# Optimization experiments

Measured on AMD Instinct MI355X. Metric: run time of the kernel, lower is better.

The kernel has to match this reference:

```python
import jax, jax.numpy as jnp
import numpy as np

N_NODES = 100000
N_EDGES = 400000
N_GRAPHS = 2500
DIM = 128
F_IN = 78
N_LAYERS = 3
BN_EPS = 1e-5


def setup_inputs() -> dict:
    key = jax.random.key(0)
    ks = jax.random.split(key, 24)
    def lin(k, fi, fo):
        return jax.random.normal(k, (fi, fo), jnp.float32) / np.sqrt(fi)
    inp = {
        "x": jax.random.normal(ks[0], (N_NODES, F_IN), jnp.float32),
        "edge_index": jax.random.randint(ks[1], (2, N_EDGES), 0, N_NODES, jnp.int32),
        "batch": jnp.sort(jax.random.randint(ks[2], (N_NODES,), 0, N_GRAPHS, jnp.int32)),
        "num_graphs": N_GRAPHS,
        "gcn1_W": lin(ks[3], F_IN, DIM), "gcn1_b": jnp.zeros((DIM,), jnp.float32),
        "gcn2_W": lin(ks[4], DIM, DIM), "gcn2_b": jnp.zeros((DIM,), jnp.float32),
        "gin0_w1": lin(ks[5], F_IN, DIM), "gin0_b1": jnp.zeros((DIM,), jnp.float32),
        "gin0_w2": lin(ks[6], DIM, DIM), "gin0_b2": jnp.zeros((DIM,), jnp.float32),
        # layers 1..2 stacked (same 128->128 shapes)
        "gin_w1": jnp.stack([lin(ks[7], DIM, DIM), lin(ks[8], DIM, DIM)]),
        "gin_b1": jnp.zeros((2, DIM), jnp.float32),
        "gin_w2": jnp.stack([lin(ks[9], DIM, DIM), lin(ks[10], DIM, DIM)]),
        "gin_b2": jnp.zeros((2, DIM), jnp.float32),
        "bn_gamma": jnp.ones((N_LAYERS, DIM), jnp.float32),
        "bn_beta": jnp.zeros((N_LAYERS, DIM), jnp.float32),
    }
    return inp


def reference(x, edge_index, batch, num_graphs,
              gcn1_W, gcn1_b, gcn2_W, gcn2_b,
              gin0_w1, gin0_b1, gin0_w2, gin0_b2,
              gin_w1, gin_b1, gin_w2, gin_b2,
              bn_gamma, bn_beta):
    n = x.shape[0]
    src, dst = edge_index[0], edge_index[1]

    def gcn(h, W, b):
        # linear -> symmetric-normalized aggregation with self loops (PyG GCNConv)
        h = h @ W
        loop = jnp.arange(n, dtype=src.dtype)
        s = jnp.concatenate([src, loop])
        d = jnp.concatenate([dst, loop])
        deg = jax.ops.segment_sum(jnp.ones(s.shape[0], h.dtype), d, num_segments=n)
        dis = jax.lax.rsqrt(deg)  # deg >= 1 thanks to self loops
        norm = (dis[s] * dis[d])[:, None]
        return jax.ops.segment_sum(h[s] * norm, d, num_segments=n) + b

    def gin(h, w1, b1, w2, b2):
        # GINConv, eps=0: mlp(x + sum_{j->i} x_j)
        agg = jax.ops.segment_sum(h[src], dst, num_segments=n)
        z = jax.nn.relu((h + agg) @ w1 + b1)
        return z @ w2 + b2

    def bn(h, g, bt):
        mu = h.mean(0)
        var = ((h - mu) ** 2).mean(0)
        return (h - mu) * jax.lax.rsqrt(var + BN_EPS) * g + bt

    g1 = jax.nn.relu(gcn(x, gcn1_W, gcn1_b))
    g2 = jax.nn.relu(gcn(g1, gcn2_W, gcn2_b))
    g2a = g2 + g1
    g2m = g2 * g1

    h = x
    xs = []
    m = jnp.float32(1.0)
    e = jnp.float32(0.0)
    for i in range(N_LAYERS):
        if i == 0:
            h = gin(h, gin0_w1, gin0_b1, gin0_w2, gin0_b2)
        else:
            h = gin(h, gin_w1[i - 1], gin_b1[i - 1], gin_w2[i - 1], gin_b2[i - 1])
        h = bn(jax.nn.relu(h), bn_gamma[i], bn_beta[i])
        m = m * h
        e = e + h
        xs.append(h)

    rep = jnp.concatenate(xs + [m, e, g1, g2, g2a, g2m], axis=-1)  # [N, 9*DIM]
    return jax.ops.segment_max(rep, batch, num_segments=num_graphs)
```

## Files before the change

### kernel.cpp

```cpp
#include <hip/hip_runtime.h>
#include <math.h>

#define DIMC 128
#define FINC 78
#define REPW 1152
#define SCAN_TILE 1024

typedef __attribute__((ext_vector_type(8))) short short8x;
typedef __attribute__((ext_vector_type(4))) float f32x4;
typedef unsigned int u32;
typedef const __attribute__((address_space(1))) u32* gas_u32p;
typedef __attribute__((address_space(3))) u32* las_u32p;

__device__ inline float b2f(unsigned short u) {
    union { unsigned int i; float f; } v; v.i = ((unsigned int)u) << 16; return v.f;
}
__device__ inline unsigned short f2b(float f) {
    union { float f; unsigned int i; } v; v.f = f;
    unsigned int r = (v.i + 0x7FFFu + ((v.i >> 16) & 1u)) >> 16;
    return (unsigned short)r;
}

__device__ __forceinline__ void gld16(const void* g, void* l) {
    __builtin_amdgcn_global_load_lds((gas_u32p)g, (las_u32p)l, 16, 0, 0);
}


__global__ void k_fill_int(int* __restrict__ p, int v, int n) {
    int i = blockIdx.x * blockDim.x + threadIdx.x;
    if (i < n) p[i] = v;
}

__global__ void k_fill(float* __restrict__ p, float v, int n) {
    int i = blockIdx.x * blockDim.x + threadIdx.x;
    if (i < n) p[i] = v;
}

__global__ void k_count(const int* __restrict__ dst, int* __restrict__ cnt, int E) {
    int e = blockIdx.x * blockDim.x + threadIdx.x;
    if (e < E) atomicAdd(&cnt[dst[e]], 1);
}

__launch_bounds__(256)
__global__ void k_tilesum(const int* __restrict__ cnt, int* __restrict__ tileSum, int N) {
    __shared__ int red[256];
    int base = blockIdx.x * SCAN_TILE;
    int s = 0;
    for (int i = threadIdx.x; i < SCAN_TILE; i += 256) {
        int idx = base + i;
        if (idx < N) s += cnt[idx];
    }
    red[threadIdx.x] = s;
    __syncthreads();
    for (int d = 128; d > 0; d >>= 1) {
        if (threadIdx.x < d) red[threadIdx.x] += red[threadIdx.x + d];
        __syncthreads();
    }
    if (threadIdx.x == 0) tileSum[blockIdx.x] = red[0];
}

__launch_bounds__(256)
__global__ void k_tilescan(const int* __restrict__ tileSum, int* __restrict__ tileOff,
                           int* __restrict__ rowptr, int T, int N) {
    __shared__ int sh[256];
    int t = threadIdx.x;
    int orig = (t < T) ? tileSum[t] : 0;
    sh[t] = orig;
    __syncthreads();
    for (int d = 1; d < 256; d <<= 1) {
        int v = (t >= d) ? sh[t - d] : 0;
        __syncthreads();
        sh[t] += v;
        __syncthreads();
    }
    if (t < T) tileOff[t] = sh[t] - orig;
    if (t == 255) rowptr[N] = sh[255];
}

__launch_bounds__(256)
__global__ void k_tileemit(const int* __restrict__ cnt, const int* __restrict__ tileOff,
                           int* __restrict__ rowptr, int* __restrict__ cursor,
                           float* __restrict__ dis, int N) {
    __shared__ int sh[256];
    int t = threadIdx.x;
    int base = blockIdx.x * SCAN_TILE;
    int idx0 = base + t * 4;
    int v0 = 0, v1 = 0, v2 = 0, v3 = 0;
    if (idx0 + 3 < N) {
        int4 v = *(const int4*)(cnt + idx0);
        v0 = v.x; v1 = v.y; v2 = v.z; v3 = v.w;
    } else {
        if (idx0 + 0 < N) v0 = cnt[idx0 + 0];
        if (idx0 + 1 < N) v1 = cnt[idx0 + 1];
        if (idx0 + 2 < N) v2 = cnt[idx0 + 2];
        if (idx0 + 3 < N) v3 = cnt[idx0 + 3];
    }
    int s0 = v0, s1 = s0 + v1, s2 = s1 + v2, s3 = s2 + v3;
    sh[t] = s3;
    __syncthreads();
    for (int d = 1; d < 256; d <<= 1) {
        int v = (t >= d) ? sh[t - d] : 0;
        __syncthreads();
        sh[t] += v;
        __syncthreads();
    }
    int gbase = tileOff[blockIdx.x] + ((t == 0) ? 0 : sh[t - 1]);
    int ex[4] = {0, s0, s1, s2};
    int vv[4] = {v0, v1, v2, v3};
#pragma unroll
    for (int j = 0; j < 4; ++j) {
        int idx = idx0 + j;
        if (idx < N) {
            int r = gbase + ex[j];
            rowptr[idx] = r;
            cursor[idx] = r;
            dis[idx] = rsqrtf((float)vv[j] + 1.0f);
        }
    }
}

__global__ void k_scatter(const int* __restrict__ src, const int* __restrict__ dst,
                          int* __restrict__ cursor, int* __restrict__ col, int E) {
    int e = blockIdx.x * blockDim.x + threadIdx.x;
    if (e < E) {
        int pos = atomicAdd(&cursor[dst[e]], 1);
        col[pos] = src[e];
    }
}

__global__ void k_bounds(const int* __restrict__ batch, int* __restrict__ start, int N, int G) {
    int g = blockIdx.x * blockDim.x + threadIdx.x;
    if (g <= G) {
        int lo = 0, hi = N;
        while (lo < hi) { int mid = (lo + hi) >> 1; if (batch[mid] < g) lo = mid + 1; else hi = mid; }
        start[g] = lo;
    }
}


__global__ void k_cvt_w(const float* __restrict__ s0, const float* __restrict__ s1,
                        const float* __restrict__ s2, const float* __restrict__ s3,
                        const float* __restrict__ s4, const float* __restrict__ s5,
                        const float* __restrict__ s6, const float* __restrict__ s7,
                        unsigned short* __restrict__ whi, unsigned short* __restrict__ wlo) {
    int my = blockIdx.y;
    const float* src; int Ksrc, KP; size_t dstoff;
    const size_t o96 = (size_t)128 * 96, o128 = (size_t)128 * 128;
    switch (my) {
        case 0: src = s0; Ksrc = 78;  KP = 96;  dstoff = 0; break;
        case 1: src = s1; Ksrc = 78;  KP = 96;  dstoff = o96; break;
        case 2: src = s2; Ksrc = 128; KP = 128; dstoff = 2 * o96; break;
        case 3: src = s3; Ksrc = 128; KP = 128; dstoff = 2 * o96 + o128; break;
        case 4: src = s4; Ksrc = 128; KP = 128; dstoff = 2 * o96 + 2 * o128; break;
        case 5: src = s5; Ksrc = 128; KP = 128; dstoff = 2 * o96 + 3 * o128; break;
        case 6: src = s6; Ksrc = 128; KP = 128; dstoff = 2 * o96 + 4 * o128; break;
        default: src = s7; Ksrc = 128; KP = 128; dstoff = 2 * o96 + 5 * o128; break;
    }
    int i = blockIdx.x * blockDim.x + threadIdx.x;
    if (i < 128 * KP) {
        int n = i / KP, k = i - n * KP;
        float v = (k < Ksrc) ? src[(size_t)k * DIMC + n] : 0.f;
        unsigned short hi = f2b(v);
        unsigned short lo = f2b(v - b2f(hi));
        whi[dstoff + i] = hi;
        wlo[dstoff + i] = lo;
    }
}


__global__ void k_pad_x(const float* __restrict__ x, float* __restrict__ x96, int N) {
    int i = blockIdx.x * blockDim.x + threadIdx.x;
    int r = i / 24, c4 = (i - r * 24) * 4;
    if (r >= N) return;
    float v[4];
#pragma unroll
    for (int j = 0; j < 4; ++j) { int k = c4 + j; v[j] = (k < FINC) ? x[(size_t)r * FINC + k] : 0.f; }
    *(float4*)(x96 + (size_t)r * 96 + c4) = make_float4(v[0], v[1], v[2], v[3]);
}


__launch_bounds__(256, 2)
__global__ void k_gemm_x2(const float* __restrict__ A,
                          const unsigned short* __restrict__ B0hi, const unsigned short* __restrict__ B0lo,
                          const unsigned short* __restrict__ B1hi, const unsigned short* __restrict__ B1lo,
                          const float* __restrict__ rowScale0,
                          float* __restrict__ C0, float* __restrict__ C1, int N) {
    constexpr int KP = 96, NC = 3;
    __shared__ float          ldsA[NC * 4096];
    __shared__ unsigned short ldsB[2][4096];
    const int tid = threadIdx.x;
    const int wave = tid >> 6, lane = tid & 63;
    const int lm = lane & 15, q = lane >> 4;
    const int wr = (wave >> 1) * 64, wc = (wave & 1) * 64;
    const int row0 = blockIdx.x * 128;

    const int au = tid & 7, ar = tid >> 3;
    const int bu = tid & 3, br = tid >> 2;

#pragma unroll
    for (int c = 0; c < NC; ++c)
#pragma unroll
        for (int p = 0; p < 4; ++p) {
            int r = p * 32 + ar;
            gld16(A + (size_t)(row0 + r) * KP + c * 32 + ((au ^ (r & 7)) << 2),
                  &ldsA[((c * 4 + p) * 256 + tid) << 2]);
        }

    const unsigned short* bh2[2] = {B0hi, B1hi};
    const unsigned short* bl2[2] = {B0lo, B1lo};

#pragma unroll
    for (int ws = 0; ws < 2; ++ws) {
        f32x4 acc[4][4];
#pragma unroll
        for (int a = 0; a < 4; ++a)
#pragma unroll
            for (int b = 0; b < 4; ++b) acc[a][b] = (f32x4){0.f, 0.f, 0.f, 0.f};

#pragma unroll
        for (int c = 0; c < NC; ++c) {
#pragma unroll
            for (int p = 0; p < 2; ++p) {
                int r = p * 64 + br;
                int so = (c << 5) + ((bu ^ ((r >> 1) & 3)) << 3);
                gld16(bh2[ws] + (size_t)r * KP + so, &ldsB[0][(p * 256 + tid) << 3]);
                gld16(bl2[ws] + (size_t)r * KP + so, &ldsB[1][(p * 256 + tid) << 3]);
            }
            asm volatile("s_waitcnt vmcnt(0)" ::: "memory");
            __builtin_amdgcn_s_barrier();
            __builtin_amdgcn_sched_barrier(0);

            short8x ah[4], al[4];
#pragma unroll
            for (int rt = 0; rt < 4; ++rt) {
                int m = wr + rt * 16 + lm;
                const float* base = &ldsA[c * 4096];
                float4 f0 = *(const float4*)&base[m * 32 + (((2 * q) ^ (m & 7)) << 2)];
                float4 f1 = *(const float4*)&base[m * 32 + ((((2 * q) + 1) ^ (m & 7)) << 2)];
                float ff[8] = {f0.x, f0.y, f0.z, f0.w, f1.x, f1.y, f1.z, f1.w};
#pragma unroll
                for (int j = 0; j < 8; ++j) {
                    unsigned short h = f2b(ff[j]);
                    ah[rt][j] = (short)h;
                    al[rt][j] = (short)f2b(ff[j] - b2f(h));
                }
            }
#pragma unroll
            for (int ct = 0; ct < 4; ++ct) {
                int n = wc + ct * 16 + lm;
                int sl = n * 32 + ((q ^ ((n >> 1) & 3)) << 3);
                short8x bh = *(const short8x*)&ldsB[0][sl];
                short8x bl = *(const short8x*)&ldsB[1][sl];
#pragma unroll
                for (int rt = 0; rt < 4; ++rt) {
                    acc[rt][ct] = __builtin_amdgcn_mfma_f32_16x16x32_bf16(bh, ah[rt], acc[rt][ct], 0, 0, 0);
                    acc[rt][ct] = __builtin_amdgcn_mfma_f32_16x16x32_bf16(bh, al[rt], acc[rt][ct], 0, 0, 0);
                    acc[rt][ct] = __builtin_amdgcn_mfma_f32_16x16x32_bf16(bl, ah[rt], acc[rt][ct], 0, 0, 0);
                }
            }
            __builtin_amdgcn_s_barrier();
        }

        float* C = ws ? C1 : C0;
#pragma unroll
        for (int rt = 0; rt < 4; ++rt) {
            int grow = row0 + wr + rt * 16 + lm;
            if (grow < N) {
                float sc = ws ? 1.f : rowScale0[grow];
#pragma unroll
                for (int ct = 0; ct < 4; ++ct) {
                    int nb = wc + ct * 16 + q * 4;
                    *(float4*)(C + (size_t)grow * DIMC + nb) =
                        make_float4(acc[rt][ct][0] * sc, acc[rt][ct][1] * sc,
                                    acc[rt][ct][2] * sc, acc[rt][ct][3] * sc);
                }
            }
        }
    }
}


template<int KP, bool STATS>
__launch_bounds__(256, 2)
__global__ void k_gemm_c(const float* __restrict__ A,
                         const unsigned short* __restrict__ Bhi,
                         const unsigned short* __restrict__ Blo,
                         const float* __restrict__ bias, const float* __restrict__ rowScale,
                         float* __restrict__ statsOut, float* __restrict__ C,
                         int N, int doRelu) {
    constexpr int NT = KP / 32;
    __shared__ float          ldsA[2][4096];
    __shared__ unsigned short ldsB[2][2][4096];
    __shared__ float sStats[256];
    const int tid = threadIdx.x;
    const int wave = tid >> 6, lane = tid & 63;
    const int lm = lane & 15, q = lane >> 4;
    const int wr = (wave >> 1) * 64, wc = (wave & 1) * 64;
    const int row0 = blockIdx.x * 128;

    const int au = tid & 7, ar = tid >> 3;
    const int bu = tid & 3, br = tid >> 2;

    auto stage = [&](int c, int d) {
        const int cb = c << 5;
#pragma unroll
        for (int p = 0; p < 4; ++p) {
            int r = p * 32 + ar;
            gld16(A + (size_t)(row0 + r) * KP + cb + ((au ^ (r & 7)) << 2),
                  &ldsA[d][(p * 256 + tid) << 2]);
        }
#pragma unroll
        for (int p = 0; p < 2; ++p) {
            int r = p * 64 + br;
            int so = cb + ((bu ^ ((r >> 1) & 3)) << 3);
            gld16(Bhi + (size_t)r * KP + so, &ldsB[d][0][(p * 256 + tid) << 3]);
            gld16(Blo + (size_t)r * KP + so, &ldsB[d][1][(p * 256 + tid) << 3]);
        }
    };

    f32x4 acc[4][4];
#pragma unroll
    for (int a = 0; a < 4; ++a)
#pragma unroll
        for (int b = 0; b < 4; ++b) acc[a][b] = (f32x4){0.f, 0.f, 0.f, 0.f};

    stage(0, 0);
#pragma unroll
    for (int t = 0; t < NT; ++t) {
        const int cur = t & 1;
        if (t + 1 < NT) {
            stage(t + 1, cur ^ 1);
            asm volatile("s_waitcnt vmcnt(8)" ::: "memory");
        } else {
            asm volatile("s_waitcnt vmcnt(0)" ::: "memory");
        }
        __builtin_amdgcn_s_barrier();
        __builtin_amdgcn_sched_barrier(0);

        short8x ah[4], al[4];
#pragma unroll
        for (int rt = 0; rt < 4; ++rt) {
            int m = wr + rt * 16 + lm;
            float4 f0 = *(const float4*)&ldsA[cur][m * 32 + (((2 * q) ^ (m & 7)) << 2)];
            float4 f1 = *(const float4*)&ldsA[cur][m * 32 + ((((2 * q) + 1) ^ (m & 7)) << 2)];
            float ff[8] = {f0.x, f0.y, f0.z, f0.w, f1.x, f1.y, f1.z, f1.w};
#pragma unroll
            for (int j = 0; j < 8; ++j) {
                unsigned short h = f2b(ff[j]);
                ah[rt][j] = (short)h;
                al[rt][j] = (short)f2b(ff[j] - b2f(h));
            }
        }
#pragma unroll
        for (int ct = 0; ct < 4; ++ct) {
            int n = wc + ct * 16 + lm;
            int sl = n * 32 + ((q ^ ((n >> 1) & 3)) << 3);
            short8x bh = *(const short8x*)&ldsB[cur][0][sl];
            short8x bl = *(const short8x*)&ldsB[cur][1][sl];
#pragma unroll
            for (int rt = 0; rt < 4; ++rt) {
                acc[rt][ct] = __builtin_amdgcn_mfma_f32_16x16x32_bf16(bh, ah[rt], acc[rt][ct], 0, 0, 0);
                acc[rt][ct] = __builtin_amdgcn_mfma_f32_16x16x32_bf16(bh, al[rt], acc[rt][ct], 0, 0, 0);
                acc[rt][ct] = __builtin_amdgcn_mfma_f32_16x16x32_bf16(bl, ah[rt], acc[rt][ct], 0, 0, 0);
            }
        }
        __builtin_amdgcn_s_barrier();
    }

    float cs[4][4], cq[4][4];
    if constexpr (STATS) {
#pragma unroll
        for (int a = 0; a < 4; ++a)
#pragma unroll
            for (int b = 0; b < 4; ++b) { cs[a][b] = 0.f; cq[a][b] = 0.f; }
    }

#pragma unroll
    for (int rt = 0; rt < 4; ++rt) {
        int grow = row0 + wr + rt * 16 + lm;
        if (grow < N) {
            float sc = rowScale ? rowScale[grow] : 1.f;
#pragma unroll
            for (int ct = 0; ct < 4; ++ct) {
                int nb = wc + ct * 16 + q * 4;
                float vv[4];
#pragma unroll
                for (int i = 0; i < 4; ++i) {
                    float v = acc[rt][ct][i];
                    if (bias) v += bias[nb + i];
                    if (doRelu) v = fmaxf(v, 0.f);
                    v *= sc;
                    vv[i] = v;
                    if constexpr (STATS) { cs[ct][i] += v; cq[ct][i] = fmaf(v, v, cq[ct][i]); }
                }
                *(float4*)(C + (size_t)grow * DIMC + nb) = make_float4(vv[0], vv[1], vv[2], vv[3]);
            }
        }
    }

    if constexpr (STATS) {
        sStats[tid] = 0.f;
        __syncthreads();
#pragma unroll
        for (int ct = 0; ct < 4; ++ct)
#pragma unroll
            for (int i = 0; i < 4; ++i) {
                float vs = cs[ct][i], vq = cq[ct][i];
#pragma unroll
                for (int o = 1; o < 16; o <<= 1) { vs += __shfl_xor(vs, o); vq += __shfl_xor(vq, o); }
                if (lm == 0) {
                    int colg = wc + ct * 16 + q * 4 + i;
                    atomicAdd(&sStats[colg], vs);
                    atomicAdd(&sStats[DIMC + colg], vq);
                }
            }
        __syncthreads();
        atomicAdd(&statsOut[tid], sStats[tid]);
    }
}


__global__ void k_bn_coef(const float* __restrict__ bnsum, const float* __restrict__ gamma,
                          const float* __restrict__ beta, float* __restrict__ coef, float invN) {
    int c = threadIdx.x;
    float mu  = bnsum[c] * invN;
    float var = bnsum[128 + c] * invN - mu * mu;
    float inv = rsqrtf(var + 1e-5f);
    float s = gamma[c] * inv;
    coef[c] = s;
    coef[128 + c] = beta[c] - mu * s;
}


__global__ void k_fold_w(const float* __restrict__ w1, const float* __restrict__ coefL,
                         unsigned short* __restrict__ fwhi, unsigned short* __restrict__ fwlo,
                         float* __restrict__ cvec) {
    __shared__ float red[128];
    int n = blockIdx.x, k = threadIdx.x;
    float w = w1[(size_t)k * DIMC + n];
    float ws = w * coefL[k];
    unsigned short h = f2b(ws);
    fwhi[(size_t)n * DIMC + k] = h;
    fwlo[(size_t)n * DIMC + k] = f2b(ws - b2f(h));
    red[k] = w * coefL[DIMC + k];
    __syncthreads();
    for (int d = 64; d > 0; d >>= 1) { if (k < d) red[k] += red[k + d]; __syncthreads(); }
    if (k == 0) cvec[n] = red[0];
}


__global__ void k_gather_gcn(const float4* __restrict__ t, const int* __restrict__ rowptr,
                             const int* __restrict__ col, const float* __restrict__ dis,
                             const float4* __restrict__ bias, float4* __restrict__ out, int N) {
    int i = blockIdx.x * blockDim.x + threadIdx.x;
    int node = i >> 5, c4 = i & 31;
    if (node >= N) return;
    int s = rowptr[node], e = rowptr[node + 1];
    float4 acc = t[(size_t)node * 32 + c4];
    for (int k = s; k < e; ++k) {
        float4 v = t[(size_t)col[k] * 32 + c4];
        acc.x += v.x; acc.y += v.y; acc.z += v.z; acc.w += v.w;
    }
    float d = dis[node];
    float4 b = bias[c4];
    float4 o;
    o.x = fmaxf(acc.x * d + b.x, 0.f);
    o.y = fmaxf(acc.y * d + b.y, 0.f);
    o.z = fmaxf(acc.z * d + b.z, 0.f);
    o.w = fmaxf(acc.w * d + b.w, 0.f);
    out[(size_t)node * 32 + c4] = o;
}

__global__ void k_gather_gin(const float4* __restrict__ t, const int* __restrict__ rowptr,
                             const int* __restrict__ col, const float4* __restrict__ bias,
                             float4* __restrict__ out, int N) {
    int i = blockIdx.x * blockDim.x + threadIdx.x;
    int node = i >> 5, c4 = i & 31;
    if (node >= N) return;
    int s = rowptr[node], e = rowptr[node + 1];
    float4 acc = t[(size_t)node * 32 + c4];
    for (int k = s; k < e; ++k) {
        float4 v = t[(size_t)col[k] * 32 + c4];
        acc.x += v.x; acc.y += v.y; acc.z += v.z; acc.w += v.w;
    }
    float4 b = bias[c4];
    float4 o;
    o.x = fmaxf(acc.x + b.x, 0.f);
    o.y = fmaxf(acc.y + b.y, 0.f);
    o.z = fmaxf(acc.z + b.z, 0.f);
    o.w = fmaxf(acc.w + b.w, 0.f);
    out[(size_t)node * 32 + c4] = o;
}


__global__ void k_segmax_gin_all(const float* __restrict__ h0, const float* __restrict__ h1,
                                 const float* __restrict__ h2, const float* __restrict__ coef,
                                 const int* __restrict__ start, float* __restrict__ out) {
    int g = blockIdx.x, c = threadIdx.x;
    float s0 = coef[c],       t0 = coef[128 + c];
    float s1 = coef[256 + c], t1 = coef[384 + c];
    float s2 = coef[512 + c], t2 = coef[640 + c];
    int s = start[g], e = start[g + 1];
    float m0 = -INFINITY, m1 = -INFINITY, m2 = -INFINITY, mm = -INFINITY, me = -INFINITY;
    for (int n = s; n < e; ++n) {
        size_t idx = (size_t)n * DIMC + c;
        float a0 = fmaf(h0[idx], s0, t0);
        float a1 = fmaf(h1[idx], s1, t1);
        float a2 = fmaf(h2[idx], s2, t2);
        m0 = fmaxf(m0, a0); m1 = fmaxf(m1, a1); m2 = fmaxf(m2, a2);
        mm = fmaxf(mm, a0 * a1 * a2);
        me = fmaxf(me, a0 + a1 + a2);
    }
    size_t o = (size_t)g * REPW + c;
    out[o]            = m0;
    out[o + 1 * DIMC] = m1;
    out[o + 2 * DIMC] = m2;
    out[o + 3 * DIMC] = mm;
    out[o + 4 * DIMC] = me;
}

__global__ void k_segmax_gcn(const float* __restrict__ G1, const float* __restrict__ G2,
                             const int* __restrict__ start, float* __restrict__ out) {
    int g = blockIdx.x, c = threadIdx.x;
    int s = start[g], e = start[g + 1];
    float m1 = -INFINITY, m2 = -INFINITY, ma = -INFINITY, mm = -INFINITY;
    for (int n = s; n < e; ++n) {
        float a = G1[(size_t)n * DIMC + c], b = G2[(size_t)n * DIMC + c];
        m1 = fmaxf(m1, a); m2 = fmaxf(m2, b);
        ma = fmaxf(ma, a + b); mm = fmaxf(mm, a * b);
    }
    size_t o = (size_t)g * REPW + c;
    out[o + 5 * DIMC] = m1;
    out[o + 6 * DIMC] = m2;
    out[o + 7 * DIMC] = ma;
    out[o + 8 * DIMC] = mm;
}


extern "C" void kernel_launch(void* const* d_in, const int* in_sizes, int n_in,
                              void* d_out, int out_size, void* d_ws, size_t ws_size,
                              hipStream_t stream) {
    const float* x       = (const float*)d_in[0];
    const int*   ei      = (const int*)d_in[1];
    const int*   batch   = (const int*)d_in[2];
    const float* gcn1_W  = (const float*)d_in[4];
    const float* gcn1_b  = (const float*)d_in[5];
    const float* gcn2_W  = (const float*)d_in[6];
    const float* gcn2_b  = (const float*)d_in[7];
    const float* gin0_w1 = (const float*)d_in[8];
    const float* gin0_b1 = (const float*)d_in[9];
    const float* gin0_w2 = (const float*)d_in[10];
    const float* gin0_b2 = (const float*)d_in[11];
    const float* gin_w1  = (const float*)d_in[12];
    const float* gin_b1  = (const float*)d_in[13];
    const float* gin_w2  = (const float*)d_in[14];
    const float* gin_b2  = (const float*)d_in[15];
    const float* bn_g    = (const float*)d_in[16];
    const float* bn_b    = (const float*)d_in[17];
    float* out = (float*)d_out;

    const int N = in_sizes[0] / FINC;
    const int E = in_sizes[1] / 2;
    const int G = out_size / REPW;
    const int* srcv = ei;
    const int* dstv = ei + E;

    char* ws = (char*)d_ws;
    size_t off = 0;
    auto alloc = [&](size_t bytes) { char* p = ws + off; off += (bytes + 255) & ~(size_t)255; return p; };
    int*   cnt     = (int*)alloc((size_t)N * 4);
    int*   rowptr  = (int*)alloc(((size_t)N + 1) * 4);
    int*   cursor  = (int*)alloc((size_t)N * 4);
    int*   col     = (int*)alloc((size_t)E * 4);
    float* dis     = (float*)alloc((size_t)N * 4);
    float* bnsum   = (float*)alloc(768 * 4);
    float* coef    = (float*)alloc(768 * 4);
    float* cvec    = (float*)alloc(128 * 4);
    int*   start   = (int*)alloc(((size_t)G + 1) * 4);
    int*   tileSum = (int*)alloc(256 * 4);
    int*   tileOff = (int*)alloc(256 * 4);
    const size_t o96 = (size_t)128 * 96, o128 = (size_t)128 * 128;
    const size_t wtElems = 2 * o96 + 6 * o128;
    unsigned short* whi  = (unsigned short*)alloc(wtElems * 2);
    unsigned short* wlo  = (unsigned short*)alloc(wtElems * 2);
    unsigned short* fwhi = (unsigned short*)alloc(o128 * 2);
    unsigned short* fwlo = (unsigned short*)alloc(o128 * 2);
    const size_t fbytes = (size_t)N * DIMC * 4;
    float* bufT = (float*)alloc(fbytes);
    float* bufZ = (float*)alloc(fbytes);
    float* h0   = (float*)alloc(fbytes);
    float* h1   = (float*)alloc(fbytes);
    float* h2   = (float*)alloc(fbytes);
    float* x96  = h1;
    (void)ws_size; (void)n_in;

    const size_t woff[8] = {0, o96, 2 * o96, 2 * o96 + o128, 2 * o96 + 2 * o128,
                            2 * o96 + 3 * o128, 2 * o96 + 4 * o128, 2 * o96 + 5 * o128};

    const int T = 256;
    auto cdiv = [](long a, long b) { return (int)((a + b - 1) / b); };
    const int gemmGrid = cdiv(N, 128);
    const int gatherGrid = cdiv((long)N * 32, T);
    const int nTiles = cdiv(N, SCAN_TILE);
    const float invN = 1.0f / (float)N;

    k_fill_int<<<cdiv(N, T), T, 0, stream>>>(cnt, 0, N);
    k_count<<<cdiv(E, T), T, 0, stream>>>(dstv, cnt, E);
    k_tilesum<<<nTiles, T, 0, stream>>>(cnt, tileSum, N);
    k_tilescan<<<1, T, 0, stream>>>(tileSum, tileOff, rowptr, nTiles, N);
    k_tileemit<<<nTiles, T, 0, stream>>>(cnt, tileOff, rowptr, cursor, dis, N);
    k_scatter<<<cdiv(E, T), T, 0, stream>>>(srcv, dstv, cursor, col, E);
    k_bounds<<<cdiv(G + 1, T), T, 0, stream>>>(batch, start, N, G);
    k_fill<<<3, T, 0, stream>>>(bnsum, 0.f, 768);
    {
        dim3 g(64, 8);
        k_cvt_w<<<g, T, 0, stream>>>(gcn1_W, gin0_w1, gcn2_W, gin0_w2,
                                     gin_w1, gin_w1 + o128, gin_w2, gin_w2 + o128, whi, wlo);
    }
    k_pad_x<<<cdiv((long)N * 24, T), T, 0, stream>>>(x, x96, N);

    k_gemm_x2<<<gemmGrid, T, 0, stream>>>(x96, whi + woff[0], wlo + woff[0],
                                          whi + woff[1], wlo + woff[1],
                                          dis, bufT, h2, N);

    k_gather_gcn<<<gatherGrid, T, 0, stream>>>((const float4*)bufT, rowptr, col, dis,
                                               (const float4*)gcn1_b, (float4*)bufZ, N);
    k_gemm_c<128, false><<<gemmGrid, T, 0, stream>>>(bufZ, whi + woff[2], wlo + woff[2],
                                                     nullptr, dis, nullptr, bufT, N, 0);
    k_gather_gcn<<<gatherGrid, T, 0, stream>>>((const float4*)bufT, rowptr, col, dis,
                                               (const float4*)gcn2_b, (float4*)h0, N);
    k_segmax_gcn<<<G, DIMC, 0, stream>>>(bufZ, h0, start, out);

    k_gather_gin<<<gatherGrid, T, 0, stream>>>((const float4*)h2, rowptr, col,
                                               (const float4*)gin0_b1, (float4*)bufZ, N);
    k_gemm_c<128, true><<<gemmGrid, T, 0, stream>>>(bufZ, whi + woff[3], wlo + woff[3],
                                                    gin0_b2, nullptr, bnsum, h0, N, 1);
    k_bn_coef<<<1, DIMC, 0, stream>>>(bnsum, bn_g, bn_b, coef, invN);
    k_fold_w<<<DIMC, DIMC, 0, stream>>>(gin_w1, coef, fwhi, fwlo, cvec);

    k_gemm_c<128, false><<<gemmGrid, T, 0, stream>>>(h0, fwhi, fwlo,
                                                     cvec, nullptr, nullptr, bufT, N, 0);
    k_gather_gin<<<gatherGrid, T, 0, stream>>>((const float4*)bufT, rowptr, col,
                                               (const float4*)gin_b1, (float4*)bufZ, N);
    k_gemm_c<128, true><<<gemmGrid, T, 0, stream>>>(bufZ, whi + woff[6], wlo + woff[6],
                                                    gin_b2, nullptr, bnsum + 256, h1, N, 1);
    k_bn_coef<<<1, DIMC, 0, stream>>>(bnsum + 256, bn_g + DIMC, bn_b + DIMC, coef + 256, invN);
    k_fold_w<<<DIMC, DIMC, 0, stream>>>(gin_w1 + o128, coef + 256, fwhi, fwlo, cvec);

    k_gemm_c<128, false><<<gemmGrid, T, 0, stream>>>(h1, fwhi, fwlo,
                                                     cvec, nullptr, nullptr, bufT, N, 0);
    k_gather_gin<<<gatherGrid, T, 0, stream>>>((const float4*)bufT, rowptr, col,
                                               (const float4*)(gin_b1 + DIMC), (float4*)bufZ, N);
    k_gemm_c<128, true><<<gemmGrid, T, 0, stream>>>(bufZ, whi + woff[7], wlo + woff[7],
                                                    gin_b2 + DIMC, nullptr, bnsum + 512, h2, N, 1);
    k_bn_coef<<<1, DIMC, 0, stream>>>(bnsum + 512, bn_g + 2 * DIMC, bn_b + 2 * DIMC, coef + 512, invN);

    k_segmax_gin_all<<<G, DIMC, 0, stream>>>(h0, h1, h2, coef, start, out);
}
```

Measured before the change: 753.2 us.

## Merge GCN and GIN-0 gathers and their follow-up GEMMs into combined launches

The first GCN gather and the GIN layer-0 gather now run in one launch, with blocks split by index between the two paths. The GCN layer-2 GEMM and the GIN-0 second GEMM run sequentially inside one kernel per row tile, and the second one writes BN statistics. This removes several launches and lets the two independent branches fill the GPU together. In exchange, buffers are reassigned: h0 is read and written in place by the GIN GEMM within the same tile, and h2 is reused to hold GCN layer-2 output. That aliasing is safe only because each block reads its own rows before writing them.

```diff
diff --git a/kernel.cpp b/kernel.cpp
--- a/kernel.cpp
+++ b/kernel.cpp
@@ -280,6 +280,164 @@
 }
 
 
+__launch_bounds__(256, 2)
+__global__ void k_gemm_d2(const float* __restrict__ A0,
+                          const unsigned short* __restrict__ B0hi, const unsigned short* __restrict__ B0lo,
+                          const float* __restrict__ rowScale0, float* __restrict__ C0,
+                          const float* __restrict__ A1,
+                          const unsigned short* __restrict__ B1hi, const unsigned short* __restrict__ B1lo,
+                          const float* __restrict__ bias1, float* __restrict__ statsOut,
+                          float* __restrict__ C1, int N) {
+    constexpr int KP = 128, NT = 4;
+    __shared__ float          ldsA[2][4096];
+    __shared__ unsigned short ldsB[2][2][4096];
+    __shared__ float sStats[256];
+    const int tid = threadIdx.x;
+    const int wave = tid >> 6, lane = tid & 63;
+    const int lm = lane & 15, q = lane >> 4;
+    const int wr = (wave >> 1) * 64, wc = (wave & 1) * 64;
+    const int row0 = blockIdx.x * 128;
+
+    const int au = tid & 7, ar = tid >> 3;
+    const int bu = tid & 3, br = tid >> 2;
+
+    const float* Aarr[2] = {A0, A1};
+    const unsigned short* Bh[2] = {B0hi, B1hi};
+    const unsigned short* Bl[2] = {B0lo, B1lo};
+
+    for (int ws = 0; ws < 2; ++ws) {
+        const float* A = Aarr[ws];
+        const unsigned short* Bhi = Bh[ws];
+        const unsigned short* Blo = Bl[ws];
+
+        auto stage = [&](int c, int d) {
+            const int cb = c << 5;
+#pragma unroll
+            for (int p = 0; p < 4; ++p) {
+                int r = p * 32 + ar;
+                gld16(A + (size_t)(row0 + r) * KP + cb + ((au ^ (r & 7)) << 2),
+                      &ldsA[d][(p * 256 + tid) << 2]);
+            }
+#pragma unroll
+            for (int p = 0; p < 2; ++p) {
+                int r = p * 64 + br;
+                int so = cb + ((bu ^ ((r >> 1) & 3)) << 3);
+                gld16(Bhi + (size_t)r * KP + so, &ldsB[d][0][(p * 256 + tid) << 3]);
+                gld16(Blo + (size_t)r * KP + so, &ldsB[d][1][(p * 256 + tid) << 3]);
+            }
+        };
+
+        f32x4 acc[4][4];
+#pragma unroll
+        for (int a = 0; a < 4; ++a)
+#pragma unroll
+            for (int b = 0; b < 4; ++b) acc[a][b] = (f32x4){0.f, 0.f, 0.f, 0.f};
+
+        stage(0, 0);
+#pragma unroll
+        for (int t = 0; t < NT; ++t) {
+            const int cur = t & 1;
+            if (t + 1 < NT) {
+                stage(t + 1, cur ^ 1);
+                asm volatile("s_waitcnt vmcnt(8)" ::: "memory");
+            } else {
+                asm volatile("s_waitcnt vmcnt(0)" ::: "memory");
+            }
+            __builtin_amdgcn_s_barrier();
+            __builtin_amdgcn_sched_barrier(0);
+
+            short8x ah[4], al[4];
+#pragma unroll
+            for (int rt = 0; rt < 4; ++rt) {
+                int m = wr + rt * 16 + lm;
+                float4 f0 = *(const float4*)&ldsA[cur][m * 32 + (((2 * q) ^ (m & 7)) << 2)];
+                float4 f1 = *(const float4*)&ldsA[cur][m * 32 + ((((2 * q) + 1) ^ (m & 7)) << 2)];
+                float ff[8] = {f0.x, f0.y, f0.z, f0.w, f1.x, f1.y, f1.z, f1.w};
+#pragma unroll
+                for (int j = 0; j < 8; ++j) {
+                    unsigned short h = f2b(ff[j]);
+                    ah[rt][j] = (short)h;
+                    al[rt][j] = (short)f2b(ff[j] - b2f(h));
+                }
+            }
+#pragma unroll
+            for (int ct = 0; ct < 4; ++ct) {
+                int n = wc + ct * 16 + lm;
+                int sl = n * 32 + ((q ^ ((n >> 1) & 3)) << 3);
+                short8x bh = *(const short8x*)&ldsB[cur][0][sl];
+                short8x bl = *(const short8x*)&ldsB[cur][1][sl];
+#pragma unroll
+                for (int rt = 0; rt < 4; ++rt) {
+                    acc[rt][ct] = __builtin_amdgcn_mfma_f32_16x16x32_bf16(bh, ah[rt], acc[rt][ct], 0, 0, 0);
+                    acc[rt][ct] = __builtin_amdgcn_mfma_f32_16x16x32_bf16(bh, al[rt], acc[rt][ct], 0, 0, 0);
+                    acc[rt][ct] = __builtin_amdgcn_mfma_f32_16x16x32_bf16(bl, ah[rt], acc[rt][ct], 0, 0, 0);
+                }
+            }
+            __builtin_amdgcn_s_barrier();
+        }
+
+        if (ws == 0) {
+#pragma unroll
+            for (int rt = 0; rt < 4; ++rt) {
+                int grow = row0 + wr + rt * 16 + lm;
+                if (grow < N) {
+                    float sc = rowScale0[grow];
+#pragma unroll
+                    for (int ct = 0; ct < 4; ++ct) {
+                        int nb = wc + ct * 16 + q * 4;
+                        *(float4*)(C0 + (size_t)grow * DIMC + nb) =
+                            make_float4(acc[rt][ct][0] * sc, acc[rt][ct][1] * sc,
+                                        acc[rt][ct][2] * sc, acc[rt][ct][3] * sc);
+                    }
+                }
+            }
+        } else {
+            float cs[4][4], cq[4][4];
+#pragma unroll
+            for (int a = 0; a < 4; ++a)
+#pragma unroll
+                for (int b = 0; b < 4; ++b) { cs[a][b] = 0.f; cq[a][b] = 0.f; }
+#pragma unroll
+            for (int rt = 0; rt < 4; ++rt) {
+                int grow = row0 + wr + rt * 16 + lm;
+                if (grow < N) {
+#pragma unroll
+                    for (int ct = 0; ct < 4; ++ct) {
+                        int nb = wc + ct * 16 + q * 4;
+                        float vv[4];
+#pragma unroll
+                        for (int i = 0; i < 4; ++i) {
+                            float v = fmaxf(acc[rt][ct][i] + bias1[nb + i], 0.f);
+                            vv[i] = v;
+                            cs[ct][i] += v; cq[ct][i] = fmaf(v, v, cq[ct][i]);
+                        }
+                        *(float4*)(C1 + (size_t)grow * DIMC + nb) =
+                            make_float4(vv[0], vv[1], vv[2], vv[3]);
+                    }
+                }
+            }
+            sStats[tid] = 0.f;
+            __syncthreads();
+#pragma unroll
+            for (int ct = 0; ct < 4; ++ct)
+#pragma unroll
+                for (int i = 0; i < 4; ++i) {
+                    float vs = cs[ct][i], vq = cq[ct][i];
+#pragma unroll
+                    for (int o = 1; o < 16; o <<= 1) { vs += __shfl_xor(vs, o); vq += __shfl_xor(vq, o); }
+                    if (lm == 0) {
+                        int colg = wc + ct * 16 + q * 4 + i;
+                        atomicAdd(&sStats[colg], vs);
+                        atomicAdd(&sStats[DIMC + colg], vq);
+                    }
+                }
+            __syncthreads();
+            atomicAdd(&statsOut[tid], sStats[tid]);
+        }
+    }
+}
+
+
 template<int KP, bool STATS>
 __launch_bounds__(256, 2)
 __global__ void k_gemm_c(const float* __restrict__ A,
@@ -448,6 +606,34 @@
     if (k == 0) cvec[n] = red[0];
 }
 
+
+__global__ void k_gather2(const float4* __restrict__ t0, const float* __restrict__ dis,
+                          const float4* __restrict__ bias0, float4* __restrict__ out0,
+                          const float4* __restrict__ t1, const float4* __restrict__ bias1,
+                          float4* __restrict__ out1,
+                          const int* __restrict__ rowptr, const int* __restrict__ col,
+                          int N, int half) {
+    int b = blockIdx.x;
+    bool gin = b >= half;
+    int i = (gin ? b - half : b) * blockDim.x + threadIdx.x;
+    int node = i >> 5, c4 = i & 31;
+    if (node >= N) return;
+    int s = rowptr[node], e = rowptr[node + 1];
+    const float4* t = gin ? t1 : t0;
+    float4 acc = t[(size_t)node * 32 + c4];
+    for (int k = s; k < e; ++k) {
+        float4 v = t[(size_t)col[k] * 32 + c4];
+        acc.x += v.x; acc.y += v.y; acc.z += v.z; acc.w += v.w;
+    }
+    float d = gin ? 1.f : dis[node];
+    float4 bb = gin ? bias1[c4] : bias0[c4];
+    float4 o;
+    o.x = fmaxf(acc.x * d + bb.x, 0.f);
+    o.y = fmaxf(acc.y * d + bb.y, 0.f);
+    o.z = fmaxf(acc.z * d + bb.z, 0.f);
+    o.w = fmaxf(acc.w * d + bb.w, 0.f);
+    (gin ? out1 : out0)[(size_t)node * 32 + c4] = o;
+}
 
 __global__ void k_gather_gcn(const float4* __restrict__ t, const int* __restrict__ rowptr,
                              const int* __restrict__ col, const float* __restrict__ dis,
@@ -623,18 +809,19 @@
                                           whi + woff[1], wlo + woff[1],
                                           dis, bufT, h2, N);
 
+    k_gather2<<<2 * gatherGrid, T, 0, stream>>>((const float4*)bufT, dis,
+                                                (const float4*)gcn1_b, (float4*)bufZ,
+                                                (const float4*)h2, (const float4*)gin0_b1,
+                                                (float4*)h0, rowptr, col, N, gatherGrid);
+
+    k_gemm_d2<<<gemmGrid, T, 0, stream>>>(bufZ, whi + woff[2], wlo + woff[2], dis, bufT,
+                                          h0, whi + woff[3], wlo + woff[3], gin0_b2,
+                                          bnsum, h0, N);
+
     k_gather_gcn<<<gatherGrid, T, 0, stream>>>((const float4*)bufT, rowptr, col, dis,
-                                               (const float4*)gcn1_b, (float4*)bufZ, N);
-    k_gemm_c<128, false><<<gemmGrid, T, 0, stream>>>(bufZ, whi + woff[2], wlo + woff[2],
-                                                     nullptr, dis, nullptr, bufT, N, 0);
-    k_gather_gcn<<<gatherGrid, T, 0, stream>>>((const float4*)bufT, rowptr, col, dis,
-                                               (const float4*)gcn2_b, (float4*)h0, N);
-    k_segmax_gcn<<<G, DIMC, 0, stream>>>(bufZ, h0, start, out);
-
-    k_gather_gin<<<gatherGrid, T, 0, stream>>>((const float4*)h2, rowptr, col,
-                                               (const float4*)gin0_b1, (float4*)bufZ, N);
-    k_gemm_c<128, true><<<gemmGrid, T, 0, stream>>>(bufZ, whi + woff[3], wlo + woff[3],
-                                                    gin0_b2, nullptr, bnsum, h0, N, 1);
+                                               (const float4*)gcn2_b, (float4*)h2, N);
+    k_segmax_gcn<<<G, DIMC, 0, stream>>>(bufZ, h2, start, out);
+
     k_bn_coef<<<1, DIMC, 0, stream>>>(bnsum, bn_g, bn_b, coef, invN);
     k_fold_w<<<DIMC, DIMC, 0, stream>>>(gin_w1, coef, fwhi, fwlo, cvec);
 
```

Measured after the change: 737.8 us. 1.02x faster.
